# Kernel optimization log

Measured on AMD Instinct MI355X. Metric: run time of the kernel, lower is better.

Reference implementation:

```python
import jax, jax.numpy as jnp
import numpy as np

DIM = 128
BATCH = 8192
# Static index sets (constants, mirror diag_ind / tril_ind / diag_ind_tril)
TRIL_R, TRIL_C = np.tril_indices(DIM)          # row/col of lower-tri entries, row-major
DIAG_IN_TRIL = np.nonzero(TRIL_R == TRIL_C)[0]  # positions of diagonal entries in flat tril vector
DIAG = np.arange(DIM)
N_TRIL = TRIL_R.size  # dim*(dim+1)/2 = 8256


def setup_inputs() -> dict:
    key = jax.random.key(0)
    x = jax.random.normal(key, (BATCH, N_TRIL), dtype=jnp.float32)
    return {"x": x}


def reference(x):
    # Scatter-fill batched lower-triangular matrix L: [..., DIM, DIM]
    batch_shape = x.shape[:-1]
    L = jnp.zeros(batch_shape + (DIM, DIM), dtype=x.dtype)
    L = L.at[..., TRIL_R, TRIL_C].set(x)
    # Overwrite diagonal with log1p(exp(x_diag) + 1e-12) (softplus-like, as in source)
    diag = jnp.log1p(jnp.exp(x[..., DIAG_IN_TRIL]) + 1e-12)
    L = L.at[..., DIAG, DIAG].set(diag)
    # Diffusion matrix L @ L^T
    return jnp.einsum('...ik,...jk->...ij', L, L)
```

## Files before the change

kernel.cpp:

```cpp
#include <hip/hip_runtime.h>
#include <math.h>


#define DIM        128
#define NTRIL      8256
#define ROW_BYTES  256

typedef __bf16 bf16x8 __attribute__((ext_vector_type(8)));
typedef float  f32x16 __attribute__((ext_vector_type(16)));

struct RcTab { unsigned short off[NTRIL]; };
static constexpr RcTab make_tab() {
    RcTab t{};
    int idx = 0;
    for (int r = 0; r < DIM; ++r)
        for (int c = 0; c <= r; ++c)
            t.off[idx++] = (unsigned short)((r * ROW_BYTES + c * 2) ^ ((r & 7) << 4));
    return t;
}
__device__ const RcTab TBL = make_tab();

__device__ __forceinline__ int rowbase(int r) {
    return (r << 8) ^ ((r & 7) << 4);
}

__global__ __launch_bounds__(256) void tril2diff_kernel(
    const float* __restrict__ x, float* __restrict__ out)
{
    __shared__ alignas(16) __bf16 Lsh[DIM * ROW_BYTES / 2];

    const int b   = blockIdx.x;
    const int tid = threadIdx.x;
    const float* xb = x + (size_t)b * NTRIL;

    float4  v[8];
    ushort4 o[8];
    #pragma unroll
    for (int i = 0; i < 8; ++i) {
        const int t4 = (tid + i * 256) * 4;
        v[i] = *(const float4*)(xb + t4);
        o[i] = *(const ushort4*)(TBL.off + t4);
    }
    float4 vt; ushort4 ot;
    if (tid < 16) {
        const int t4 = (2048 + tid) * 4;
        vt = *(const float4*)(xb + t4);
        ot = *(const ushort4*)(TBL.off + t4);
    }
    float dvx;
    if (tid < DIM)
        dvx = xb[(tid * (tid + 1)) / 2 + tid];

    uint4* lz4 = (uint4*)Lsh;
    #pragma unroll
    for (int i = 0; i < 8; ++i)
        lz4[tid + i * 256] = uint4{0u, 0u, 0u, 0u};
    __syncthreads();

    char* lbw = (char*)Lsh;
    #pragma unroll
    for (int i = 0; i < 8; ++i) {
        *(__bf16*)(lbw + o[i].x) = (__bf16)v[i].x;
        *(__bf16*)(lbw + o[i].y) = (__bf16)v[i].y;
        *(__bf16*)(lbw + o[i].z) = (__bf16)v[i].z;
        *(__bf16*)(lbw + o[i].w) = (__bf16)v[i].w;
    }
    if (tid < 16) {
        *(__bf16*)(lbw + ot.x) = (__bf16)vt.x;
        *(__bf16*)(lbw + ot.y) = (__bf16)vt.y;
        *(__bf16*)(lbw + ot.z) = (__bf16)vt.z;
        *(__bf16*)(lbw + ot.w) = (__bf16)vt.w;
    }
    float dv;
    if (tid < DIM)
        dv = log1pf(expf(dvx) + 1e-12f);
    __syncthreads();

    if (tid < DIM)
        *(__bf16*)(lbw + ((tid * ROW_BYTES + tid * 2) ^ ((tid & 7) << 4))) = (__bf16)dv;
    __syncthreads();

    const int lane = tid & 63;
    const int wv   = tid >> 6;
    const int i0   = (wv >> 1) * 64;
    const int j0   = (wv & 1) * 64;
    const int cl   = lane & 31;
    const int hh   = lane >> 5;
    const int kb   = hh * 16;

    const int ba0 = rowbase(i0      + cl);
    const int ba1 = rowbase(i0 + 32 + cl);
    const int bb0 = rowbase(j0      + cl);
    const int bb1 = rowbase(j0 + 32 + cl);

    f32x16 acc00 = {0}, acc01 = {0}, acc10 = {0}, acc11 = {0};
    const char* lb = (const char*)Lsh;

#define MFMA_STEP(ks)                                                          \
    {                                                                          \
        const int koff = (ks) * 32 + kb;                                       \
        bf16x8 a0 = *(const bf16x8*)(lb + (ba0 ^ koff));                       \
        bf16x8 a1 = *(const bf16x8*)(lb + (ba1 ^ koff));                       \
        bf16x8 b0 = *(const bf16x8*)(lb + (bb0 ^ koff));                       \
        bf16x8 b1 = *(const bf16x8*)(lb + (bb1 ^ koff));                       \
        acc00 = __builtin_amdgcn_mfma_f32_32x32x16_bf16(a0, b0, acc00, 0, 0, 0); \
        acc01 = __builtin_amdgcn_mfma_f32_32x32x16_bf16(a0, b1, acc01, 0, 0, 0); \
        acc10 = __builtin_amdgcn_mfma_f32_32x32x16_bf16(a1, b0, acc10, 0, 0, 0); \
        acc11 = __builtin_amdgcn_mfma_f32_32x32x16_bf16(a1, b1, acc11, 0, 0, 0); \
    }

    #pragma unroll
    for (int ks = 0; ks < 4; ++ks)
        MFMA_STEP(ks);
    if (wv == 3) {
        #pragma unroll
        for (int ks = 4; ks < 8; ++ks)
            MFMA_STEP(ks);
    }
#undef MFMA_STEP

    float* ob = out + (size_t)b * (DIM * DIM);
    #pragma unroll
    for (int reg = 0; reg < 16; ++reg) {
        const int row = (reg & 3) + 8 * (reg >> 2) + 4 * hh;
        ob[(i0      + row) * DIM + j0      + cl] = acc00[reg];
        ob[(i0      + row) * DIM + j0 + 32 + cl] = acc01[reg];
        ob[(i0 + 32 + row) * DIM + j0      + cl] = acc10[reg];
        ob[(i0 + 32 + row) * DIM + j0 + 32 + cl] = acc11[reg];
    }
}

extern "C" void kernel_launch(void* const* d_in, const int* in_sizes, int n_in,
                              void* d_out, int out_size, void* d_ws, size_t ws_size,
                              hipStream_t stream) {
    const float* x = (const float*)d_in[0];
    float* out = (float*)d_out;
    const int batch = in_sizes[0] / NTRIL;
    tril2diff_kernel<<<batch, 256, 0, stream>>>(x, out);
}
```

Before: 680.7 us.

## Process four batch matrices per block and prefetch the next input during MFMA

Each block now handles NB=4 consecutive batch elements instead of one. It loads the next element's tril values into registers while the current one is multiplied and written out. The offset table is loaded and shared memory is zeroed once per block, so that fixed cost is spread over four elements. The trade-offs are a quarter as many blocks, an extra barrier per iteration, and higher register pressure from keeping the prefetched data live across the MFMA loop.

New measurement: 683.6 us. No clear change (+0.4%).

```diff
diff --git a/kernel.cpp b/kernel.cpp
--- a/kernel.cpp
+++ b/kernel.cpp
@@ -5,6 +5,7 @@
 #define DIM        128
 #define NTRIL      8256
 #define ROW_BYTES  256
+#define NB         4
 
 typedef __bf16 bf16x8 __attribute__((ext_vector_type(8)));
 typedef float  f32x16 __attribute__((ext_vector_type(16)));
@@ -29,55 +30,33 @@
 {
     __shared__ alignas(16) __bf16 Lsh[DIM * ROW_BYTES / 2];
 
-    const int b   = blockIdx.x;
     const int tid = threadIdx.x;
-    const float* xb = x + (size_t)b * NTRIL;
+    const int b0  = blockIdx.x * NB;
 
-    float4  v[8];
-    ushort4 o[8];
+    ushort4 o[8], ot;
     #pragma unroll
-    for (int i = 0; i < 8; ++i) {
-        const int t4 = (tid + i * 256) * 4;
-        v[i] = *(const float4*)(xb + t4);
-        o[i] = *(const ushort4*)(TBL.off + t4);
+    for (int i = 0; i < 8; ++i)
+        o[i] = *(const ushort4*)(TBL.off + (tid + i * 256) * 4);
+    if (tid < 16)
+        ot = *(const ushort4*)(TBL.off + (2048 + tid) * 4);
+
+    float4 v[8], vt;
+    float  dvx;
+    {
+        const float* xb = x + (size_t)b0 * NTRIL;
+        #pragma unroll
+        for (int i = 0; i < 8; ++i)
+            v[i] = *(const float4*)(xb + (tid + i * 256) * 4);
+        if (tid < 16)
+            vt = *(const float4*)(xb + (2048 + tid) * 4);
+        if (tid < DIM)
+            dvx = xb[(tid * (tid + 1)) / 2 + tid];
     }
-    float4 vt; ushort4 ot;
-    if (tid < 16) {
-        const int t4 = (2048 + tid) * 4;
-        vt = *(const float4*)(xb + t4);
-        ot = *(const ushort4*)(TBL.off + t4);
-    }
-    float dvx;
-    if (tid < DIM)
-        dvx = xb[(tid * (tid + 1)) / 2 + tid];
 
     uint4* lz4 = (uint4*)Lsh;
     #pragma unroll
     for (int i = 0; i < 8; ++i)
         lz4[tid + i * 256] = uint4{0u, 0u, 0u, 0u};
-    __syncthreads();
-
-    char* lbw = (char*)Lsh;
-    #pragma unroll
-    for (int i = 0; i < 8; ++i) {
-        *(__bf16*)(lbw + o[i].x) = (__bf16)v[i].x;
-        *(__bf16*)(lbw + o[i].y) = (__bf16)v[i].y;
-        *(__bf16*)(lbw + o[i].z) = (__bf16)v[i].z;
-        *(__bf16*)(lbw + o[i].w) = (__bf16)v[i].w;
-    }
-    if (tid < 16) {
-        *(__bf16*)(lbw + ot.x) = (__bf16)vt.x;
-        *(__bf16*)(lbw + ot.y) = (__bf16)vt.y;
-        *(__bf16*)(lbw + ot.z) = (__bf16)vt.z;
-        *(__bf16*)(lbw + ot.w) = (__bf16)vt.w;
-    }
-    float dv;
-    if (tid < DIM)
-        dv = log1pf(expf(dvx) + 1e-12f);
-    __syncthreads();
-
-    if (tid < DIM)
-        *(__bf16*)(lbw + ((tid * ROW_BYTES + tid * 2) ^ ((tid & 7) << 4))) = (__bf16)dv;
     __syncthreads();
 
     const int lane = tid & 63;
@@ -87,14 +66,49 @@
     const int cl   = lane & 31;
     const int hh   = lane >> 5;
     const int kb   = hh * 16;
-
     const int ba0 = rowbase(i0      + cl);
     const int ba1 = rowbase(i0 + 32 + cl);
     const int bb0 = rowbase(j0      + cl);
     const int bb1 = rowbase(j0 + 32 + cl);
 
-    f32x16 acc00 = {0}, acc01 = {0}, acc10 = {0}, acc11 = {0};
-    const char* lb = (const char*)Lsh;
+    char*       lbw = (char*)Lsh;
+    const char* lb  = (const char*)Lsh;
+
+    for (int n = 0; n < NB; ++n) {
+        #pragma unroll
+        for (int i = 0; i < 8; ++i) {
+            *(__bf16*)(lbw + o[i].x) = (__bf16)v[i].x;
+            *(__bf16*)(lbw + o[i].y) = (__bf16)v[i].y;
+            *(__bf16*)(lbw + o[i].z) = (__bf16)v[i].z;
+            *(__bf16*)(lbw + o[i].w) = (__bf16)v[i].w;
+        }
+        if (tid < 16) {
+            *(__bf16*)(lbw + ot.x) = (__bf16)vt.x;
+            *(__bf16*)(lbw + ot.y) = (__bf16)vt.y;
+            *(__bf16*)(lbw + ot.z) = (__bf16)vt.z;
+            *(__bf16*)(lbw + ot.w) = (__bf16)vt.w;
+        }
+        float dv;
+        if (tid < DIM)
+            dv = log1pf(expf(dvx) + 1e-12f);
+        __syncthreads();
+
+        if (tid < DIM)
+            *(__bf16*)(lbw + ((tid * ROW_BYTES + tid * 2) ^ ((tid & 7) << 4))) = (__bf16)dv;
+        __syncthreads();
+
+        if (n + 1 < NB) {
+            const float* xb = x + (size_t)(b0 + n + 1) * NTRIL;
+            #pragma unroll
+            for (int i = 0; i < 8; ++i)
+                v[i] = *(const float4*)(xb + (tid + i * 256) * 4);
+            if (tid < 16)
+                vt = *(const float4*)(xb + (2048 + tid) * 4);
+            if (tid < DIM)
+                dvx = xb[(tid * (tid + 1)) / 2 + tid];
+        }
+
+        f32x16 acc00 = {0}, acc01 = {0}, acc10 = {0}, acc11 = {0};
 
 #define MFMA_STEP(ks)                                                          \
     {                                                                          \
@@ -109,24 +123,27 @@
         acc11 = __builtin_amdgcn_mfma_f32_32x32x16_bf16(a1, b1, acc11, 0, 0, 0); \
     }
 
-    #pragma unroll
-    for (int ks = 0; ks < 4; ++ks)
-        MFMA_STEP(ks);
-    if (wv == 3) {
         #pragma unroll
-        for (int ks = 4; ks < 8; ++ks)
+        for (int ks = 0; ks < 4; ++ks)
             MFMA_STEP(ks);
-    }
+        if (wv == 3) {
+            #pragma unroll
+            for (int ks = 4; ks < 8; ++ks)
+                MFMA_STEP(ks);
+        }
 #undef MFMA_STEP
 
-    float* ob = out + (size_t)b * (DIM * DIM);
-    #pragma unroll
-    for (int reg = 0; reg < 16; ++reg) {
-        const int row = (reg & 3) + 8 * (reg >> 2) + 4 * hh;
-        ob[(i0      + row) * DIM + j0      + cl] = acc00[reg];
-        ob[(i0      + row) * DIM + j0 + 32 + cl] = acc01[reg];
-        ob[(i0 + 32 + row) * DIM + j0      + cl] = acc10[reg];
-        ob[(i0 + 32 + row) * DIM + j0 + 32 + cl] = acc11[reg];
+        __syncthreads();
+
+        float* ob = out + (size_t)(b0 + n) * (DIM * DIM);
+        #pragma unroll
+        for (int reg = 0; reg < 16; ++reg) {
+            const int row = (reg & 3) + 8 * (reg >> 2) + 4 * hh;
+            ob[(i0      + row) * DIM + j0      + cl] = acc00[reg];
+            ob[(i0      + row) * DIM + j0 + 32 + cl] = acc01[reg];
+            ob[(i0 + 32 + row) * DIM + j0      + cl] = acc10[reg];
+            ob[(i0 + 32 + row) * DIM + j0 + 32 + cl] = acc11[reg];
+        }
     }
 }
 
@@ -136,5 +153,5 @@
     const float* x = (const float*)d_in[0];
     float* out = (float*)d_out;
     const int batch = in_sizes[0] / NTRIL;
-    tril2diff_kernel<<<batch, 256, 0, stream>>>(x, out);
+    tril2diff_kernel<<<batch / NB, 256, 0, stream>>>(x, out);
 }
```
